# Performance work log

Measured on AMD Instinct MI355X. Metric: run time of the kernel, lower is better.

The kernel has to match this reference:

```python
import jax, jax.numpy as jnp
import numpy as np

N = 100000   # num_nodes
F_IN = 128   # num_features
D = 64       # encoder_dim
E = 1600000  # num raw edges (avg degree 16)
BETA = 0.01  # perturb_value


def setup_inputs() -> dict:
    key = jax.random.key(0)
    ks = jax.random.split(key, 8)
    x = jax.random.normal(ks[0], (N, F_IN), dtype=jnp.float32)
    edge_index = jax.random.randint(ks[1], (2, E), 0, N, dtype=jnp.int64)
    W1 = jax.random.normal(ks[2], (F_IN, D), dtype=jnp.float32) * 0.05
    b1 = jnp.zeros((D,), dtype=jnp.float32)
    W2 = jax.random.normal(ks[3], (D, D), dtype=jnp.float32) * 0.05
    b2 = jnp.zeros((D,), dtype=jnp.float32)
    # torch FloatTensor(...).normal_(-beta, beta): mean=-beta, std=beta
    perturb1 = jax.random.normal(ks[4], (N, D), dtype=jnp.float32) * BETA - BETA
    perturb2 = jax.random.normal(ks[5], (N, D), dtype=jnp.float32) * BETA - BETA
    return {"x": x, "edge_index": edge_index, "W1": W1, "b1": b1,
            "W2": W2, "b2": b2, "perturb1": perturb1, "perturb2": perturb2}


def _graph_conv(h, src, dst, norm, W, b):
    # linear transform then gather -> weighted message -> scatter-add
    h = h @ W                                  # [N, D]
    msg = h[src] * norm[:, None]               # [E+N, D] irregular gather
    agg = jax.ops.segment_sum(msg, dst, num_segments=N)  # scatter-add
    return agg + b


def reference(x, edge_index, W1, b1, W2, b2, perturb1, perturb2):
    # add self-loops (GCN/PPMI-style propagation with symmetric norm;
    # PPMI edge weights approximated by degree normalization)
    loops = jnp.arange(N, dtype=edge_index.dtype)
    src = jnp.concatenate([edge_index[0], loops])
    dst = jnp.concatenate([edge_index[1], loops])
    deg = jax.ops.segment_sum(jnp.ones_like(dst, dtype=x.dtype), dst, num_segments=N)
    deg = jnp.maximum(deg, 1.0)
    norm = jax.lax.rsqrt(deg[src] * deg[dst])  # [E+N]

    h = _graph_conv(x, src, dst, norm, W1, b1) + perturb1
    h = jax.nn.relu(h)                         # dropout = identity (eval mode)
    h = _graph_conv(h, src, dst, norm, W2, b2) + perturb2
    return h
```

## Files before the change

kernel.cpp:

```cpp
#include <hip/hip_runtime.h>

#define DD 64
#define FIN 128
#define BK 256
#define MAXBUK 512
#define CAP 8192
#define ESCAP 12288
#define EPB 4096

typedef _Float16 half8 __attribute__((ext_vector_type(8)));
typedef _Float16 h2 __attribute__((ext_vector_type(2)));
typedef float f32x4 __attribute__((ext_vector_type(4)));

union U4 { uint4 u; h2 h[4]; };

__global__ __launch_bounds__(256) void k_bucket(const int* __restrict__ src,
                                                const int* __restrict__ dst,
                                                unsigned* __restrict__ buf,
                                                int* __restrict__ gcur,
                                                int E, int nbuk) {
    __shared__ int hist[MAXBUK];
    __shared__ int base[MAXBUK];
    int e0 = blockIdx.x * EPB;
    int e1 = min(e0 + EPB, E);
    int dreg[16];
#pragma unroll
    for (int i = 0; i < 16; ++i) {
        int e = e0 + threadIdx.x + i * 256;
        dreg[i] = (e < e1) ? dst[e] : -1;
    }
    for (int i = threadIdx.x; i < nbuk; i += 256) hist[i] = 0;
    __syncthreads();
#pragma unroll
    for (int i = 0; i < 16; ++i)
        if (dreg[i] >= 0) atomicAdd(&hist[dreg[i] >> 8], 1);
    __syncthreads();
    for (int i = threadIdx.x; i < nbuk; i += 256) {
        int c = hist[i];
        base[i] = c ? atomicAdd(&gcur[i], c) : 0;
        hist[i] = 0;
    }
    __syncthreads();
#pragma unroll
    for (int i = 0; i < 16; ++i) {
        int d = dreg[i];
        if (d >= 0) {
            int e = e0 + threadIdx.x + i * 256;
            int b = d >> 8;
            int off = base[b] + atomicAdd(&hist[b], 1);
            if (off < CAP)
                buf[(size_t)b * CAP + off] = ((unsigned)src[e] << 8) | ((unsigned)d & 255u);
        }
    }
}

__global__ __launch_bounds__(256) void k_csr(const unsigned* __restrict__ buf,
                                             const int* __restrict__ gcur,
                                             int* __restrict__ rowptr,
                                             int* __restrict__ lenp,
                                             float* __restrict__ rs,
                                             int* __restrict__ es, int n, int dummy) {
    __shared__ int cnt[BK];
    __shared__ int excl[BK];
    __shared__ int cur[BK];
    __shared__ int wsum[4];
    int b = blockIdx.x;
    int tid = threadIdx.x;
    int lane = tid & 63, wid = tid >> 6;
    cnt[tid] = 0;
    cur[tid] = 0;
    __syncthreads();
    int count = gcur[b];
    const unsigned* rec = buf + (size_t)b * CAP;
    for (int i = tid; i < count; i += 256)
        atomicAdd(&cnt[rec[i] & (BK - 1)], 1);
    __syncthreads();
    int v = cnt[tid];
    int pv = (v + 15) & ~15;
    int s = pv;
    for (int off = 1; off < 64; off <<= 1) {
        int t = __shfl_up(s, off, 64);
        if (lane >= off) s += t;
    }
    if (lane == 63) wsum[wid] = s;
    __syncthreads();
    int wo = 0;
    for (int w = 0; w < wid; ++w) wo += wsum[w];
    excl[tid] = s - pv + wo;
    __syncthreads();
    int node = b * BK + tid;
    int base = b * ESCAP;
    if (node < n) {
        rowptr[node] = base + excl[tid];
        lenp[node] = pv;
        rs[node] = rsqrtf((float)(v + 1));
    }
    for (int i = tid; i < count; i += 256) {
        unsigned r = rec[i];
        int local = r & (BK - 1);
        int pos = base + excl[local] + atomicAdd(&cur[local], 1);
        es[pos] = (int)(r >> 8);
    }
    int st = base + excl[tid];
    for (int i = v; i < pv; ++i) es[st + i] = dummy;
}

__global__ __launch_bounds__(256) void k_prep(const float* __restrict__ W1,
                                              const float* __restrict__ W2,
                                              _Float16* __restrict__ Wt1,
                                              _Float16* __restrict__ Wt2,
                                              int* __restrict__ gcur) {
    int tid = threadIdx.x;
    gcur[tid] = 0;
    gcur[tid + 256] = 0;
    for (int i = tid; i < FIN * DD; i += 256) {
        int k = i >> 6, c = i & 63;
        Wt1[c * FIN + k] = (_Float16)W1[i];
    }
    for (int i = tid; i < DD * DD; i += 256) {
        int k = i >> 6, c = i & 63;
        Wt2[c * DD + k] = (_Float16)W2[i];
    }
}

__global__ __launch_bounds__(256) void k_gemm1(const float* __restrict__ x,
                                               const _Float16* __restrict__ Wt,
                                               const float* __restrict__ rs,
                                               _Float16* __restrict__ hpf, int n) {
    __shared__ _Float16 sx[64 * 136];
    int row0 = blockIdx.x * 64;
    int tid = threadIdx.x;
    for (int i = tid; i < 2048; i += 256) {
        int r = i >> 5, c = i & 31;
        int row = row0 + r;
        float4 v = make_float4(0.f, 0.f, 0.f, 0.f);
        if (row < n) v = *(const float4*)(x + (size_t)row * FIN + c * 4);
        union { _Float16 h[4]; uint2 u; } t;
        t.h[0] = (_Float16)v.x; t.h[1] = (_Float16)v.y;
        t.h[2] = (_Float16)v.z; t.h[3] = (_Float16)v.w;
        *(uint2*)(sx + r * 136 + c * 4) = t.u;
    }
    __syncthreads();
    int lane = tid & 63, wave = tid >> 6;
    int r15 = lane & 15, g = lane >> 4;
    half8 a[4];
    const _Float16* ap = sx + (wave * 16 + r15) * 136 + g * 8;
#pragma unroll
    for (int kc = 0; kc < 4; ++kc) a[kc] = *(const half8*)(ap + kc * 32);
    half8 bfr[4][4];
    const _Float16* bp = Wt + (size_t)r15 * FIN + g * 8;
#pragma unroll
    for (int ct = 0; ct < 4; ++ct)
#pragma unroll
        for (int kc = 0; kc < 4; ++kc)
            bfr[ct][kc] = *(const half8*)(bp + ct * 16 * FIN + kc * 32);
    f32x4 acc[4] = {{0.f,0.f,0.f,0.f},{0.f,0.f,0.f,0.f},{0.f,0.f,0.f,0.f},{0.f,0.f,0.f,0.f}};
#pragma unroll
    for (int ct = 0; ct < 4; ++ct)
#pragma unroll
        for (int kc = 0; kc < 4; ++kc)
            acc[ct] = __builtin_amdgcn_mfma_f32_16x16x32_f16(a[kc], bfr[ct][kc], acc[ct], 0, 0, 0);
    __syncthreads();
#pragma unroll
    for (int reg = 0; reg < 4; ++reg) {
        int rowl = wave * 16 + g * 4 + reg;
        int row = row0 + rowl;
        float sc = (row < n) ? rs[row] : 0.f;
#pragma unroll
        for (int ct = 0; ct < 4; ++ct)
            sx[rowl * 72 + ct * 16 + r15] = (_Float16)(acc[ct][reg] * sc);
    }
    __syncthreads();
    for (int i = tid; i < 1024; i += 256) {
        int r = i >> 4, q = i & 15;
        uint2 v = *(const uint2*)(sx + r * 72 + q * 4);
        *(uint2*)(hpf + (size_t)(row0 + r) * DD + q * 4) = v;
    }
}

__global__ __launch_bounds__(256) void k_gemm2(const _Float16* __restrict__ ain,
                                               const _Float16* __restrict__ Wt,
                                               const float* __restrict__ rs,
                                               _Float16* __restrict__ hpf, int n) {
    __shared__ _Float16 sx[64 * 72];
    int row0 = blockIdx.x * 64;
    int tid = threadIdx.x;
    for (int i = tid; i < 512; i += 256) {
        int r = i >> 3, c = i & 7;
        int row = row0 + r;
        uint4 v = make_uint4(0u, 0u, 0u, 0u);
        if (row < n) v = *(const uint4*)(ain + (size_t)row * DD + c * 8);
        *(uint4*)(sx + r * 72 + c * 8) = v;
    }
    __syncthreads();
    int lane = tid & 63, wave = tid >> 6;
    int r15 = lane & 15, g = lane >> 4;
    half8 a[2];
    const _Float16* ap = sx + (wave * 16 + r15) * 72 + g * 8;
#pragma unroll
    for (int kc = 0; kc < 2; ++kc) a[kc] = *(const half8*)(ap + kc * 32);
    half8 bfr[4][2];
    const _Float16* bp = Wt + (size_t)r15 * DD + g * 8;
#pragma unroll
    for (int ct = 0; ct < 4; ++ct)
#pragma unroll
        for (int kc = 0; kc < 2; ++kc)
            bfr[ct][kc] = *(const half8*)(bp + ct * 16 * DD + kc * 32);
    f32x4 acc[4] = {{0.f,0.f,0.f,0.f},{0.f,0.f,0.f,0.f},{0.f,0.f,0.f,0.f},{0.f,0.f,0.f,0.f}};
#pragma unroll
    for (int ct = 0; ct < 4; ++ct)
#pragma unroll
        for (int kc = 0; kc < 2; ++kc)
            acc[ct] = __builtin_amdgcn_mfma_f32_16x16x32_f16(a[kc], bfr[ct][kc], acc[ct], 0, 0, 0);
    __syncthreads();
#pragma unroll
    for (int reg = 0; reg < 4; ++reg) {
        int rowl = wave * 16 + g * 4 + reg;
        int row = row0 + rowl;
        float sc = (row < n) ? rs[row] : 0.f;
#pragma unroll
        for (int ct = 0; ct < 4; ++ct)
            sx[rowl * 72 + ct * 16 + r15] = (_Float16)(acc[ct][reg] * sc);
    }
    __syncthreads();
    for (int i = tid; i < 1024; i += 256) {
        int r = i >> 4, q = i & 15;
        uint2 v = *(const uint2*)(sx + r * 72 + q * 4);
        *(uint2*)(hpf + (size_t)(row0 + r) * DD + q * 4) = v;
    }
}

template <bool F16OUT>
__global__ __launch_bounds__(256) void k_agg(const uint4* __restrict__ hp4,
                                             const int* __restrict__ es,
                                             const int* __restrict__ rowptr,
                                             const int* __restrict__ lenp,
                                             const float* __restrict__ rs,
                                             const float* __restrict__ b,
                                             const float* __restrict__ pert,
                                             float* __restrict__ outp,
                                             _Float16* __restrict__ outh, int n) {
    int lane = threadIdx.x & 63;
    int wv = threadIdx.x >> 6;
    int g = lane >> 4;
    int sub = lane & 15;
    int eslot = sub >> 3;
    int q = sub & 7;
    int node = (blockIdx.x * 4 + wv) * 4 + g;
    bool alive = node < n;
    int nc = alive ? node : 0;
    int e0 = rowptr[nc];
    int len = alive ? lenp[nc] : 0;
    int nbt = len >> 4;
    h2 A[4] = {{0,0},{0,0},{0,0},{0,0}};
    h2 B[4] = {{0,0},{0,0},{0,0},{0,0}};
    h2 C[4] = {{0,0},{0,0},{0,0},{0,0}};
    h2 D[4] = {{0,0},{0,0},{0,0},{0,0}};
    if (alive && eslot == 0) {
        U4 t; t.u = hp4[(size_t)nc * 8 + q];
        A[0] += t.h[0]; A[1] += t.h[1]; A[2] += t.h[2]; A[3] += t.h[3];
    }
    int idx = nbt ? es[e0 + sub] : 0;
    for (int t = 0; t < nbt; ++t) {
        int pa = (t + 1 < nbt) ? (e0 + (t + 1) * 16 + sub) : (e0 + sub);
        int idxn = nbt ? es[pa] : 0;
        int i0 = __shfl(idx, 0 + eslot, 16);
        int i1 = __shfl(idx, 2 + eslot, 16);
        int i2 = __shfl(idx, 4 + eslot, 16);
        int i3 = __shfl(idx, 6 + eslot, 16);
        int i4 = __shfl(idx, 8 + eslot, 16);
        int i5 = __shfl(idx, 10 + eslot, 16);
        int i6 = __shfl(idx, 12 + eslot, 16);
        int i7 = __shfl(idx, 14 + eslot, 16);
        U4 v0, v1, v2, v3, v4, v5, v6, v7;
        v0.u = hp4[(size_t)i0 * 8 + q];
        v1.u = hp4[(size_t)i1 * 8 + q];
        v2.u = hp4[(size_t)i2 * 8 + q];
        v3.u = hp4[(size_t)i3 * 8 + q];
        v4.u = hp4[(size_t)i4 * 8 + q];
        v5.u = hp4[(size_t)i5 * 8 + q];
        v6.u = hp4[(size_t)i6 * 8 + q];
        v7.u = hp4[(size_t)i7 * 8 + q];
#pragma unroll
        for (int k = 0; k < 4; ++k) {
            A[k] += v0.h[k]; B[k] += v1.h[k]; C[k] += v2.h[k]; D[k] += v3.h[k];
            A[k] += v4.h[k]; B[k] += v5.h[k]; C[k] += v6.h[k]; D[k] += v7.h[k];
        }
        idx = idxn;
    }
    float F[8];
#pragma unroll
    for (int k = 0; k < 4; ++k) {
        F[2 * k]     = ((float)A[k].x + (float)B[k].x) + ((float)C[k].x + (float)D[k].x);
        F[2 * k + 1] = ((float)A[k].y + (float)B[k].y) + ((float)C[k].y + (float)D[k].y);
    }
#pragma unroll
    for (int j = 0; j < 8; ++j)
        F[j] += __shfl_xor(F[j], 8, 64);
    if (alive && eslot == 0) {
        float r = rs[nc];
        size_t o = (size_t)nc * DD + q * 8;
        float4 p0 = *(const float4*)(pert + o);
        float4 p1 = *(const float4*)(pert + o + 4);
        float4 b0 = *(const float4*)(b + q * 8);
        float4 b1 = *(const float4*)(b + q * 8 + 4);
        float r0 = fmaf(r, F[0], b0.x + p0.x);
        float r1 = fmaf(r, F[1], b0.y + p0.y);
        float r2 = fmaf(r, F[2], b0.z + p0.z);
        float r3 = fmaf(r, F[3], b0.w + p0.w);
        float r4 = fmaf(r, F[4], b1.x + p1.x);
        float r5 = fmaf(r, F[5], b1.y + p1.y);
        float r6 = fmaf(r, F[6], b1.z + p1.z);
        float r7 = fmaf(r, F[7], b1.w + p1.w);
        if (F16OUT) {
            union { _Float16 h[8]; uint4 u; } t;
            t.h[0] = (_Float16)fmaxf(r0, 0.f);
            t.h[1] = (_Float16)fmaxf(r1, 0.f);
            t.h[2] = (_Float16)fmaxf(r2, 0.f);
            t.h[3] = (_Float16)fmaxf(r3, 0.f);
            t.h[4] = (_Float16)fmaxf(r4, 0.f);
            t.h[5] = (_Float16)fmaxf(r5, 0.f);
            t.h[6] = (_Float16)fmaxf(r6, 0.f);
            t.h[7] = (_Float16)fmaxf(r7, 0.f);
            *(uint4*)(outh + o) = t.u;
        } else {
            *(float4*)(outp + o) = make_float4(r0, r1, r2, r3);
            *(float4*)(outp + o + 4) = make_float4(r4, r5, r6, r7);
        }
    }
}

extern "C" void kernel_launch(void* const* d_in, const int* in_sizes, int n_in,
                              void* d_out, int out_size, void* d_ws, size_t ws_size,
                              hipStream_t stream) {
    const float* x  = (const float*)d_in[0];
    const int*   ei = (const int*)d_in[1];
    const float* W1 = (const float*)d_in[2];
    const float* b1 = (const float*)d_in[3];
    const float* W2 = (const float*)d_in[4];
    const float* b2 = (const float*)d_in[5];
    const float* p1 = (const float*)d_in[6];
    const float* p2 = (const float*)d_in[7];
    float* out = (float*)d_out;

    int n = in_sizes[0] / FIN;
    int E = in_sizes[1] / 2;
    const int* src = ei;
    const int* dst = ei + E;
    int nbuk = (n + BK - 1) / BK;
    int gb = (n + 63) / 64;

    char* ws = (char*)d_ws;
    size_t off = 0;
    int* gcur   = (int*)(ws + off); off += sizeof(int) * MAXBUK;
    int* rowptr = (int*)(ws + off); off += sizeof(int) * (size_t)n;
    int* lenp   = (int*)(ws + off); off += sizeof(int) * (size_t)n;
    float* rs   = (float*)(ws + off); off += sizeof(float) * (size_t)n;
    int* es     = (int*)(ws + off); off += sizeof(int) * (size_t)nbuk * ESCAP;
    off = (off + 15) & ~(size_t)15;
    unsigned* buf = (unsigned*)(ws + off);
    off += sizeof(unsigned) * (size_t)nbuk * CAP;
    off = (off + 15) & ~(size_t)15;
    _Float16* hpf = (_Float16*)(ws + off);
    off += (size_t)gb * 64 * DD * 2;
    off = (off + 15) & ~(size_t)15;
    _Float16* hpf2 = (_Float16*)(ws + off);
    off += (size_t)gb * 64 * DD * 2;
    off = (off + 15) & ~(size_t)15;
    _Float16* Wt1 = (_Float16*)(ws + off); off += FIN * DD * 2;
    _Float16* Wt2 = (_Float16*)(ws + off); off += DD * DD * 2;

    int ab = (n + 15) / 16;
    int bb = (E + EPB - 1) / EPB;

    k_prep<<<1, 256, 0, stream>>>(W1, W2, Wt1, Wt2, gcur);
    k_bucket<<<bb, 256, 0, stream>>>(src, dst, buf, gcur, E, nbuk);
    k_csr<<<nbuk, 256, 0, stream>>>(buf, gcur, rowptr, lenp, rs, es, n, n);

    k_gemm1<<<gb, 256, 0, stream>>>(x, Wt1, rs, hpf, n);
    k_agg<true><<<ab, 256, 0, stream>>>((const uint4*)hpf, es, rowptr, lenp, rs,
                                        b1, p1, nullptr, hpf2, n);
    k_gemm2<<<gb, 256, 0, stream>>>(hpf2, Wt2, rs, hpf, n);
    k_agg<false><<<ab, 256, 0, stream>>>((const uint4*)hpf, es, rowptr, lenp, rs,
                                         b2, p2, out, nullptr, n);
}
```

Before: 163.3 us.

## Sort nodes by padded degree within buckets to balance aggregation wavefronts

The CSR build kernel now counting-sorts the 256 nodes of each bucket by their padded 16-edge batch count (capped at 16) and writes a node permutation. The aggregation kernels read their node id through this order array, so the four nodes sharing a wavefront have similar loop trip counts and less divergence. It costs an extra histogram, scan and write in the CSR kernel, an extra indirect load per node, and scattered output writes. Nodes past n in the last bucket are kept in the order array and masked off by the existing alive check.

```diff
diff --git a/kernel.cpp b/kernel.cpp
--- a/kernel.cpp
+++ b/kernel.cpp
@@ -59,16 +59,20 @@
                                              int* __restrict__ rowptr,
                                              int* __restrict__ lenp,
                                              float* __restrict__ rs,
-                                             int* __restrict__ es, int n, int dummy) {
+                                             int* __restrict__ es,
+                                             int* __restrict__ order,
+                                             int n, int dummy) {
     __shared__ int cnt[BK];
     __shared__ int excl[BK];
     __shared__ int cur[BK];
     __shared__ int wsum[4];
+    __shared__ int h17[24], e17[24], c17[24];
     int b = blockIdx.x;
     int tid = threadIdx.x;
     int lane = tid & 63, wid = tid >> 6;
     cnt[tid] = 0;
     cur[tid] = 0;
+    if (tid < 24) { h17[tid] = 0; c17[tid] = 0; }
     __syncthreads();
     int count = gcur[b];
     const unsigned* rec = buf + (size_t)b * CAP;
@@ -95,11 +99,21 @@
         lenp[node] = pv;
         rs[node] = rsqrtf((float)(v + 1));
     }
+    int nbt = min(pv >> 4, 16);
+    atomicAdd(&h17[nbt], 1);
+    __syncthreads();
+    if (tid == 0) {
+        int acc = 0;
+        for (int k = 0; k < 17; ++k) { e17[k] = acc; acc += h17[k]; }
+    }
+    __syncthreads();
+    int pos = e17[nbt] + atomicAdd(&c17[nbt], 1);
+    order[b * BK + pos] = node;
     for (int i = tid; i < count; i += 256) {
         unsigned r = rec[i];
         int local = r & (BK - 1);
-        int pos = base + excl[local] + atomicAdd(&cur[local], 1);
-        es[pos] = (int)(r >> 8);
+        int p = base + excl[local] + atomicAdd(&cur[local], 1);
+        es[p] = (int)(r >> 8);
     }
     int st = base + excl[tid];
     for (int i = v; i < pv; ++i) es[st + i] = dummy;
@@ -235,6 +249,7 @@
                                              const int* __restrict__ es,
                                              const int* __restrict__ rowptr,
                                              const int* __restrict__ lenp,
+                                             const int* __restrict__ order,
                                              const float* __restrict__ rs,
                                              const float* __restrict__ b,
                                              const float* __restrict__ pert,
@@ -246,7 +261,7 @@
     int sub = lane & 15;
     int eslot = sub >> 3;
     int q = sub & 7;
-    int node = (blockIdx.x * 4 + wv) * 4 + g;
+    int node = order[(blockIdx.x * 4 + wv) * 4 + g];
     bool alive = node < n;
     int nc = alive ? node : 0;
     int e0 = rowptr[nc];
@@ -356,6 +371,7 @@
     int* rowptr = (int*)(ws + off); off += sizeof(int) * (size_t)n;
     int* lenp   = (int*)(ws + off); off += sizeof(int) * (size_t)n;
     float* rs   = (float*)(ws + off); off += sizeof(float) * (size_t)n;
+    int* order  = (int*)(ws + off); off += sizeof(int) * (size_t)nbuk * BK;
     int* es     = (int*)(ws + off); off += sizeof(int) * (size_t)nbuk * ESCAP;
     off = (off + 15) & ~(size_t)15;
     unsigned* buf = (unsigned*)(ws + off);
@@ -370,17 +386,17 @@
     _Float16* Wt1 = (_Float16*)(ws + off); off += FIN * DD * 2;
     _Float16* Wt2 = (_Float16*)(ws + off); off += DD * DD * 2;
 
-    int ab = (n + 15) / 16;
+    int ab = (nbuk * BK) / 16;
     int bb = (E + EPB - 1) / EPB;
 
     k_prep<<<1, 256, 0, stream>>>(W1, W2, Wt1, Wt2, gcur);
     k_bucket<<<bb, 256, 0, stream>>>(src, dst, buf, gcur, E, nbuk);
-    k_csr<<<nbuk, 256, 0, stream>>>(buf, gcur, rowptr, lenp, rs, es, n, n);
+    k_csr<<<nbuk, 256, 0, stream>>>(buf, gcur, rowptr, lenp, rs, es, order, n, n);
 
     k_gemm1<<<gb, 256, 0, stream>>>(x, Wt1, rs, hpf, n);
-    k_agg<true><<<ab, 256, 0, stream>>>((const uint4*)hpf, es, rowptr, lenp, rs,
-                                        b1, p1, nullptr, hpf2, n);
+    k_agg<true><<<ab, 256, 0, stream>>>((const uint4*)hpf, es, rowptr, lenp, order,
+                                        rs, b1, p1, nullptr, hpf2, n);
     k_gemm2<<<gb, 256, 0, stream>>>(hpf2, Wt2, rs, hpf, n);
-    k_agg<false><<<ab, 256, 0, stream>>>((const uint4*)hpf, es, rowptr, lenp, rs,
-                                         b2, p2, out, nullptr, n);
-}
+    k_agg<false><<<ab, 256, 0, stream>>>((const uint4*)hpf, es, rowptr, lenp, order,
+                                         rs, b2, p2, out, nullptr, n);
+}
```

After: 164.9 us. Within noise of the previous version (+1.0%).

## Map one 8-lane group per node in aggregation, removing cross-slot reduction

Applied to the files above, without the earlier changes.

The aggregation kernel now gives each node 8 lanes (one per 16-byte feature chunk) instead of 16 lanes split into two edge slots. Each iteration loads 16 edge indices with a vectorized uint2 read and broadcasts them by shuffle, then issues 16 gathers per lane. This removes the final cross-slot shuffle reduction and the prefetch logic. The epilogue loads for bias and perturbation are hoisted ahead of the loop, and the grid is halved because each block now covers 32 nodes. The trade-off is fewer lanes per node, more registers for the 16 in-flight gathers, and no prefetch of the next batch of indices.

```diff
diff --git a/kernel.cpp b/kernel.cpp
--- a/kernel.cpp
+++ b/kernel.cpp
@@ -242,68 +242,70 @@
                                              _Float16* __restrict__ outh, int n) {
     int lane = threadIdx.x & 63;
     int wv = threadIdx.x >> 6;
-    int g = lane >> 4;
-    int sub = lane & 15;
-    int eslot = sub >> 3;
-    int q = sub & 7;
-    int node = (blockIdx.x * 4 + wv) * 4 + g;
+    int q = lane & 7;
+    int g = lane >> 3;
+    int node = (blockIdx.x * 4 + wv) * 8 + g;
     bool alive = node < n;
     int nc = alive ? node : 0;
     int e0 = rowptr[nc];
     int len = alive ? lenp[nc] : 0;
     int nbt = len >> 4;
+    float r = rs[nc];
+    size_t o = (size_t)nc * DD + q * 8;
+    float4 p0 = *(const float4*)(pert + o);
+    float4 p1 = *(const float4*)(pert + o + 4);
+    float4 b0 = *(const float4*)(b + q * 8);
+    float4 b1 = *(const float4*)(b + q * 8 + 4);
     h2 A[4] = {{0,0},{0,0},{0,0},{0,0}};
     h2 B[4] = {{0,0},{0,0},{0,0},{0,0}};
     h2 C[4] = {{0,0},{0,0},{0,0},{0,0}};
     h2 D[4] = {{0,0},{0,0},{0,0},{0,0}};
-    if (alive && eslot == 0) {
+    {
         U4 t; t.u = hp4[(size_t)nc * 8 + q];
         A[0] += t.h[0]; A[1] += t.h[1]; A[2] += t.h[2]; A[3] += t.h[3];
     }
-    int idx = nbt ? es[e0 + sub] : 0;
     for (int t = 0; t < nbt; ++t) {
-        int pa = (t + 1 < nbt) ? (e0 + (t + 1) * 16 + sub) : (e0 + sub);
-        int idxn = nbt ? es[pa] : 0;
-        int i0 = __shfl(idx, 0 + eslot, 16);
-        int i1 = __shfl(idx, 2 + eslot, 16);
-        int i2 = __shfl(idx, 4 + eslot, 16);
-        int i3 = __shfl(idx, 6 + eslot, 16);
-        int i4 = __shfl(idx, 8 + eslot, 16);
-        int i5 = __shfl(idx, 10 + eslot, 16);
-        int i6 = __shfl(idx, 12 + eslot, 16);
-        int i7 = __shfl(idx, 14 + eslot, 16);
-        U4 v0, v1, v2, v3, v4, v5, v6, v7;
-        v0.u = hp4[(size_t)i0 * 8 + q];
-        v1.u = hp4[(size_t)i1 * 8 + q];
-        v2.u = hp4[(size_t)i2 * 8 + q];
-        v3.u = hp4[(size_t)i3 * 8 + q];
-        v4.u = hp4[(size_t)i4 * 8 + q];
-        v5.u = hp4[(size_t)i5 * 8 + q];
-        v6.u = hp4[(size_t)i6 * 8 + q];
-        v7.u = hp4[(size_t)i7 * 8 + q];
+        uint2 eb = *(const uint2*)(es + e0 + t * 16 + q * 2);
+        int j0  = __shfl((int)eb.x, 0, 8), j1  = __shfl((int)eb.y, 0, 8);
+        int j2  = __shfl((int)eb.x, 1, 8), j3  = __shfl((int)eb.y, 1, 8);
+        int j4  = __shfl((int)eb.x, 2, 8), j5  = __shfl((int)eb.y, 2, 8);
+        int j6  = __shfl((int)eb.x, 3, 8), j7  = __shfl((int)eb.y, 3, 8);
+        int j8  = __shfl((int)eb.x, 4, 8), j9  = __shfl((int)eb.y, 4, 8);
+        int j10 = __shfl((int)eb.x, 5, 8), j11 = __shfl((int)eb.y, 5, 8);
+        int j12 = __shfl((int)eb.x, 6, 8), j13 = __shfl((int)eb.y, 6, 8);
+        int j14 = __shfl((int)eb.x, 7, 8), j15 = __shfl((int)eb.y, 7, 8);
+        U4 v0, v1, v2, v3, v4, v5, v6, v7, v8, v9, v10, v11, v12, v13, v14, v15;
+        v0.u  = hp4[(size_t)j0  * 8 + q];
+        v1.u  = hp4[(size_t)j1  * 8 + q];
+        v2.u  = hp4[(size_t)j2  * 8 + q];
+        v3.u  = hp4[(size_t)j3  * 8 + q];
+        v4.u  = hp4[(size_t)j4  * 8 + q];
+        v5.u  = hp4[(size_t)j5  * 8 + q];
+        v6.u  = hp4[(size_t)j6  * 8 + q];
+        v7.u  = hp4[(size_t)j7  * 8 + q];
+        v8.u  = hp4[(size_t)j8  * 8 + q];
+        v9.u  = hp4[(size_t)j9  * 8 + q];
+        v10.u = hp4[(size_t)j10 * 8 + q];
+        v11.u = hp4[(size_t)j11 * 8 + q];
+        v12.u = hp4[(size_t)j12 * 8 + q];
+        v13.u = hp4[(size_t)j13 * 8 + q];
+        v14.u = hp4[(size_t)j14 * 8 + q];
+        v15.u = hp4[(size_t)j15 * 8 + q];
 #pragma unroll
         for (int k = 0; k < 4; ++k) {
-            A[k] += v0.h[k]; B[k] += v1.h[k]; C[k] += v2.h[k]; D[k] += v3.h[k];
-            A[k] += v4.h[k]; B[k] += v5.h[k]; C[k] += v6.h[k]; D[k] += v7.h[k];
+            A[k] += v0.h[k];  B[k] += v1.h[k];  C[k] += v2.h[k];  D[k] += v3.h[k];
+            A[k] += v4.h[k];  B[k] += v5.h[k];  C[k] += v6.h[k];  D[k] += v7.h[k];
+            A[k] += v8.h[k];  B[k] += v9.h[k];  C[k] += v10.h[k]; D[k] += v11.h[k];
+            A[k] += v12.h[k]; B[k] += v13.h[k]; C[k] += v14.h[k]; D[k] += v15.h[k];
         }
-        idx = idxn;
-    }
-    float F[8];
-#pragma unroll
-    for (int k = 0; k < 4; ++k) {
-        F[2 * k]     = ((float)A[k].x + (float)B[k].x) + ((float)C[k].x + (float)D[k].x);
-        F[2 * k + 1] = ((float)A[k].y + (float)B[k].y) + ((float)C[k].y + (float)D[k].y);
-    }
-#pragma unroll
-    for (int j = 0; j < 8; ++j)
-        F[j] += __shfl_xor(F[j], 8, 64);
-    if (alive && eslot == 0) {
-        float r = rs[nc];
-        size_t o = (size_t)nc * DD + q * 8;
-        float4 p0 = *(const float4*)(pert + o);
-        float4 p1 = *(const float4*)(pert + o + 4);
-        float4 b0 = *(const float4*)(b + q * 8);
-        float4 b1 = *(const float4*)(b + q * 8 + 4);
+    }
+    if (alive) {
+        float F[8];
+#pragma unroll
+        for (int k = 0; k < 4; ++k) {
+            F[2 * k]     = ((float)A[k].x + (float)B[k].x) + ((float)C[k].x + (float)D[k].x);
+            F[2 * k + 1] = ((float)A[k].y + (float)B[k].y) + ((float)C[k].y + (float)D[k].y);
+        }
         float r0 = fmaf(r, F[0], b0.x + p0.x);
         float r1 = fmaf(r, F[1], b0.y + p0.y);
         float r2 = fmaf(r, F[2], b0.z + p0.z);
@@ -370,7 +372,7 @@
     _Float16* Wt1 = (_Float16*)(ws + off); off += FIN * DD * 2;
     _Float16* Wt2 = (_Float16*)(ws + off); off += DD * DD * 2;
 
-    int ab = (n + 15) / 16;
+    int ab = (n + 31) / 32;
     int bb = (E + EPB - 1) / EPB;
 
     k_prep<<<1, 256, 0, stream>>>(W1, W2, Wt1, Wt2, gcur);
```

Measured after the change: 168.9 us. 1.03x slower.
